# Kernel optimization log

Measured on AMD Instinct MI355X. Metric: run time of the kernel, lower is better.

Reference implementation:

```python
import jax, jax.numpy as jnp
import numpy as np

H = 64  # hidden_size hardcoded in the module


def _lstm_scan(x_pre, w_hh):
    # x_pre: [T, B, 4H] = x @ W_ih^T + b_ih + b_hh, precomputed for all steps
    # w_hh: [4H, H]. PyTorch gate order: i, f, g, o.
    B = x_pre.shape[1]
    h0 = jnp.zeros((B, H), x_pre.dtype)
    c0 = jnp.zeros((B, H), x_pre.dtype)

    def cell(carry, xp):
        h, c = carry
        gates = xp + h @ w_hh.T  # [B, 4H]
        i, f, g, o = jnp.split(gates, 4, axis=-1)
        i = jax.nn.sigmoid(i)
        f = jax.nn.sigmoid(f)
        g = jnp.tanh(g)
        o = jax.nn.sigmoid(o)
        c = f * c + i * g
        h = o * jnp.tanh(c)
        return (h, c), h

    _, hs = jax.lax.scan(cell, (h0, c0), x_pre)
    return hs  # [T, B, H]


def _bidir_layer(x, w_ih, w_hh, b_ih, b_hh):
    # x: [T, B, D]; w_ih: [2, 4H, D]; w_hh: [2, 4H, H]; b_*: [2, 4H]
    pre_f = jnp.einsum('tbd,gd->tbg', x, w_ih[0]) + b_ih[0] + b_hh[0]
    hs_f = _lstm_scan(pre_f, w_hh[0])
    xr = x[::-1]
    pre_b = jnp.einsum('tbd,gd->tbg', xr, w_ih[1]) + b_ih[1] + b_hh[1]
    hs_b = _lstm_scan(pre_b, w_hh[1])[::-1]  # re-reverse to align with time
    return jnp.concatenate([hs_f, hs_b], axis=-1)  # [T, B, 2H]


def setup_inputs() -> dict:
    key = jax.random.key(0)
    B, T, F = 1024, 512, 32
    ks = jax.random.split(key, 11)
    s = 1.0 / float(np.sqrt(H))  # PyTorch LSTM init: U(-1/sqrt(H), 1/sqrt(H))
    u = lambda k, shape: jax.random.uniform(k, shape, jnp.float32, -s, s)
    return dict(
        x=jax.random.normal(ks[0], (B, T, F), jnp.float32),
        w_ih0=u(ks[1], (2, 4 * H, F)),
        w_hh0=u(ks[2], (2, 4 * H, H)),
        b_ih0=u(ks[3], (2, 4 * H)),
        b_hh0=u(ks[4], (2, 4 * H)),
        w_ih1=u(ks[5], (2, 4 * H, 2 * H)),
        w_hh1=u(ks[6], (2, 4 * H, H)),
        b_ih1=u(ks[7], (2, 4 * H)),
        b_hh1=u(ks[8], (2, 4 * H)),
        fc_w=u(ks[9], (2, 2 * H)),
        fc_b=u(ks[10], (2,)),
    )


def reference(x, w_ih0, w_hh0, b_ih0, b_hh0, w_ih1, w_hh1, b_ih1, b_hh1, fc_w, fc_b):
    xt = jnp.transpose(x, (1, 0, 2))  # [T, B, F]
    h1 = _bidir_layer(xt, w_ih0, w_hh0, b_ih0, b_hh0)  # [T, B, 2H]
    h2 = _bidir_layer(h1, w_ih1, w_hh1, b_ih1, b_hh1)  # [T, B, 2H]
    last = h2[-1]  # out[:, -1, :] in batch_first layout -> [B, 2H]
    return last @ fc_w.T + fc_b  # [B, 2]
```

## Files before the change

kernel.cpp:

```cpp
#include <hip/hip_runtime.h>

#define TT 512
#define BB 1024
#define FF 32
#define HH 64
#define GG 256

__device__ float g_h1[(size_t)TT * BB * 2 * HH];
__device__ float g_pre0[(size_t)2 * TT * BB * GG];
__device__ float g_pre1[(size_t)TT * BB * GG];
__device__ float g_hf[(size_t)BB * HH];

__device__ __forceinline__ float fsigm(float x) {
    float e = __builtin_amdgcn_exp2f(x * -1.44269504088896f);
    return __builtin_amdgcn_rcpf(1.0f + e);
}
__device__ __forceinline__ float ftanh(float x) {
    float e = __builtin_amdgcn_exp2f(x * -2.88539008177793f);
    return 2.0f * __builtin_amdgcn_rcpf(1.0f + e) - 1.0f;
}
__device__ __forceinline__ float rlane(float v, int l) {
    return __int_as_float(__builtin_amdgcn_readlane(__float_as_int(v), l));
}

__global__ __launch_bounds__(256, 4) void pre_gemm0(
    const float* __restrict__ x,
    const float* __restrict__ w_ih,
    const float* __restrict__ b_ih,
    const float* __restrict__ b_hh)
{
    const int tid = threadIdx.x;
    const int b   = blockIdx.x >> 1;
    const int dir = blockIdx.x & 1;

    __shared__ __align__(16) float4 w4[8 * 256];
    __shared__ __align__(16) float xbuf[2][256];

    const float4* wsrc = (const float4*)(w_ih + ((size_t)dir * GG + tid) * FF);
#pragma unroll
    for (int kq = 0; kq < 8; ++kq) w4[kq * 256 + tid] = wsrc[kq];
    const float bias = b_ih[dir * GG + tid] + b_hh[dir * GG + tid];

    const float* xbase = x + (size_t)b * TT * FF;
    xbuf[0][tid] = xbase[tid];
    const size_t OS = (size_t)BB * GG;

    for (int tc = 0; tc < 64; ++tc) {
        const int cur = tc & 1;
        __syncthreads();

        float vnext = 0.f;
        if (tc + 1 < 64) vnext = xbase[(tc + 1) * 256 + tid];

        float a0 = bias, a1 = bias, a2 = bias, a3 = bias,
              a4 = bias, a5 = bias, a6 = bias, a7 = bias;
#pragma unroll
        for (int kq = 0; kq < 8; ++kq) {
            float4 wq = w4[kq * 256 + tid];
            const float4* xr = (const float4*)xbuf[cur];
            float4 q;
            q = xr[0 * 8 + kq]; a0 += q.x*wq.x + q.y*wq.y + q.z*wq.z + q.w*wq.w;
            q = xr[1 * 8 + kq]; a1 += q.x*wq.x + q.y*wq.y + q.z*wq.z + q.w*wq.w;
            q = xr[2 * 8 + kq]; a2 += q.x*wq.x + q.y*wq.y + q.z*wq.z + q.w*wq.w;
            q = xr[3 * 8 + kq]; a3 += q.x*wq.x + q.y*wq.y + q.z*wq.z + q.w*wq.w;
            q = xr[4 * 8 + kq]; a4 += q.x*wq.x + q.y*wq.y + q.z*wq.z + q.w*wq.w;
            q = xr[5 * 8 + kq]; a5 += q.x*wq.x + q.y*wq.y + q.z*wq.z + q.w*wq.w;
            q = xr[6 * 8 + kq]; a6 += q.x*wq.x + q.y*wq.y + q.z*wq.z + q.w*wq.w;
            q = xr[7 * 8 + kq]; a7 += q.x*wq.x + q.y*wq.y + q.z*wq.z + q.w*wq.w;
        }
        float* op = g_pre0 + (((size_t)dir * TT + tc * 8) * BB + b) * GG + tid;
        op[0] = a0; op[1 * OS] = a1; op[2 * OS] = a2; op[3 * OS] = a3;
        op[4 * OS] = a4; op[5 * OS] = a5; op[6 * OS] = a6; op[7 * OS] = a7;

        if (tc + 1 < 64) xbuf[1 - cur][tid] = vnext;
    }
}

template <int L>
__global__ __attribute__((amdgpu_flat_work_group_size(64, 64),
                          amdgpu_waves_per_eu(1, 1)))
void lstm_scan(
    const float* __restrict__ w_hh)
{
    const int l   = threadIdx.x;
    const int dir = (L == 0) ? (blockIdx.x & 1) : 0;
    const int b   = (L == 0) ? (int)(blockIdx.x >> 1) : (int)blockIdx.x;

    const float* wbase = w_hh + (size_t)dir * GG * HH;

    float4 wi[16], wf[16], wg[16], wo[16];
    {
        const float4* pi_ = (const float4*)(wbase + (size_t)(0   + l) * HH);
        const float4* pf_ = (const float4*)(wbase + (size_t)(64  + l) * HH);
        const float4* pg_ = (const float4*)(wbase + (size_t)(128 + l) * HH);
        const float4* po_ = (const float4*)(wbase + (size_t)(192 + l) * HH);
#pragma unroll
        for (int q = 0; q < 16; ++q) {
            wi[q] = pi_[q]; wf[q] = pf_[q]; wg[q] = pg_[q]; wo[q] = po_[q];
        }
    }

    const float* pre = (L == 0) ? (g_pre0 + (size_t)dir * TT * BB * GG) : g_pre1;

    float c = 0.f, h = 0.f;

    const int t0 = dir ? (TT - 1) : 0;
    const int t1 = dir ? (TT - 2) : 1;
    const float* pp0 = pre + ((size_t)t0 * BB + b) * GG;
    const float* pp1 = pre + ((size_t)t1 * BB + b) * GG;
    float ci0 = pp0[l], cf0 = pp0[64 + l], cg0 = pp0[128 + l], co0 = pp0[192 + l];
    float ci1 = pp1[l], cf1 = pp1[64 + l], cg1 = pp1[128 + l], co1 = pp1[192 + l];

#pragma unroll 2
    for (int s = 0; s < TT; ++s) {
        const int t = dir ? (TT - 1 - s) : s;

        float ni = 0.f, nf = 0.f, ng = 0.f, no_ = 0.f;
        if (s + 2 < TT) {
            const int tn = dir ? (TT - 3 - s) : (s + 2);
            const float* np = pre + ((size_t)tn * BB + b) * GG;
            ni = np[l]; nf = np[64 + l]; ng = np[128 + l]; no_ = np[192 + l];
        }

        float ai = ci0, af = cf0, ag = cg0, ao = co0;

#define STEPQ(q) do {                                                        \
        float s0 = rlane(h, 4*(q)+0), s1 = rlane(h, 4*(q)+1),                \
              s2 = rlane(h, 4*(q)+2), s3 = rlane(h, 4*(q)+3);                \
        ai += s0*wi[q].x + s1*wi[q].y + s2*wi[q].z + s3*wi[q].w;             \
        af += s0*wf[q].x + s1*wf[q].y + s2*wf[q].z + s3*wf[q].w;             \
        ag += s0*wg[q].x + s1*wg[q].y + s2*wg[q].z + s3*wg[q].w;             \
        ao += s0*wo[q].x + s1*wo[q].y + s2*wo[q].z + s3*wo[q].w;             \
    } while (0)

        STEPQ(0);  STEPQ(1);  STEPQ(2);  STEPQ(3);
        STEPQ(4);  STEPQ(5);  STEPQ(6);  STEPQ(7);
        STEPQ(8);  STEPQ(9);  STEPQ(10); STEPQ(11);
        STEPQ(12); STEPQ(13); STEPQ(14); STEPQ(15);
#undef STEPQ

        const float ig = fsigm(ai);
        const float fg = fsigm(af);
        const float gg = ftanh(ag);
        const float og = fsigm(ao);
        c = fg * c + ig * gg;
        h = og * ftanh(c);

        if (L == 0) {
            g_h1[((size_t)t * BB + b) * (2 * HH) + dir * HH + l] = h;
        } else {
            if (s == TT - 1) g_hf[(size_t)b * HH + l] = h;
        }

        ci0 = ci1; cf0 = cf1; cg0 = cg1; co0 = co1;
        ci1 = ni;  cf1 = nf;  cg1 = ng;  co1 = no_;
    }
}

__global__ __launch_bounds__(256, 2) void pre_gemm1(
    const float* __restrict__ w_ih,
    const float* __restrict__ b_ih,
    const float* __restrict__ b_hh)
{
    const int tid  = threadIdx.x;
    const int gl   = tid & 127;
    const int rg   = tid >> 7;
    const int b    = blockIdx.x >> 1;
    const int gate = (blockIdx.x & 1) * 128 + gl;

    __shared__ __align__(16) float4 w4[28 * 128];
    __shared__ __align__(16) float4 hstg[2][8 * 32];

    const float4* wsrc = (const float4*)w_ih + (size_t)gate * 32;
#pragma unroll
    for (int i = 0; i < 14; ++i) {
        int kq = rg * 14 + i;
        w4[kq * 128 + gl] = wsrc[kq];
    }
    float4 wr0 = wsrc[28], wr1 = wsrc[29], wr2 = wsrc[30], wr3 = wsrc[31];
    const float bias = b_ih[gate] + b_hh[gate];

    const int srow = tid >> 5, sq = tid & 31;
    hstg[0][srow * 32 + sq] =
        *((const float4*)(g_h1 + ((size_t)srow * BB + b) * 128) + sq);

    const size_t RS = (size_t)BB * GG;

    for (int tc = 0; tc < 64; ++tc) {
        const int cur = tc & 1;
        __syncthreads();

        float4 vnext = make_float4(0.f, 0.f, 0.f, 0.f);
        if (tc + 1 < 64)
            vnext = *((const float4*)(g_h1 +
                      ((size_t)((tc + 1) * 8 + srow) * BB + b) * 128) + sq);

        const float4* hr0 = &hstg[cur][(rg * 4 + 0) * 32];
        const float4* hr1 = &hstg[cur][(rg * 4 + 1) * 32];
        const float4* hr2 = &hstg[cur][(rg * 4 + 2) * 32];
        const float4* hr3 = &hstg[cur][(rg * 4 + 3) * 32];

        float a0 = bias, a1 = bias, a2 = bias, a3 = bias;
#pragma unroll
        for (int kq = 0; kq < 28; ++kq) {
            float4 wq = w4[kq * 128 + gl];
            float4 q;
            q = hr0[kq]; a0 += q.x*wq.x + q.y*wq.y + q.z*wq.z + q.w*wq.w;
            q = hr1[kq]; a1 += q.x*wq.x + q.y*wq.y + q.z*wq.z + q.w*wq.w;
            q = hr2[kq]; a2 += q.x*wq.x + q.y*wq.y + q.z*wq.z + q.w*wq.w;
            q = hr3[kq]; a3 += q.x*wq.x + q.y*wq.y + q.z*wq.z + q.w*wq.w;
        }
        {
            float4 q;
            q = hr0[28]; a0 += q.x*wr0.x + q.y*wr0.y + q.z*wr0.z + q.w*wr0.w;
            q = hr1[28]; a1 += q.x*wr0.x + q.y*wr0.y + q.z*wr0.z + q.w*wr0.w;
            q = hr2[28]; a2 += q.x*wr0.x + q.y*wr0.y + q.z*wr0.z + q.w*wr0.w;
            q = hr3[28]; a3 += q.x*wr0.x + q.y*wr0.y + q.z*wr0.z + q.w*wr0.w;
            q = hr0[29]; a0 += q.x*wr1.x + q.y*wr1.y + q.z*wr1.z + q.w*wr1.w;
            q = hr1[29]; a1 += q.x*wr1.x + q.y*wr1.y + q.z*wr1.z + q.w*wr1.w;
            q = hr2[29]; a2 += q.x*wr1.x + q.y*wr1.y + q.z*wr1.z + q.w*wr1.w;
            q = hr3[29]; a3 += q.x*wr1.x + q.y*wr1.y + q.z*wr1.z + q.w*wr1.w;
            q = hr0[30]; a0 += q.x*wr2.x + q.y*wr2.y + q.z*wr2.z + q.w*wr2.w;
            q = hr1[30]; a1 += q.x*wr2.x + q.y*wr2.y + q.z*wr2.z + q.w*wr2.w;
            q = hr2[30]; a2 += q.x*wr2.x + q.y*wr2.y + q.z*wr2.z + q.w*wr2.w;
            q = hr3[30]; a3 += q.x*wr2.x + q.y*wr2.y + q.z*wr2.z + q.w*wr2.w;
            q = hr0[31]; a0 += q.x*wr3.x + q.y*wr3.y + q.z*wr3.z + q.w*wr3.w;
            q = hr1[31]; a1 += q.x*wr3.x + q.y*wr3.y + q.z*wr3.z + q.w*wr3.w;
            q = hr2[31]; a2 += q.x*wr3.x + q.y*wr3.y + q.z*wr3.z + q.w*wr3.w;
            q = hr3[31]; a3 += q.x*wr3.x + q.y*wr3.y + q.z*wr3.z + q.w*wr3.w;
        }
        {
            const int tb = tc * 8 + rg * 4;
            float* op = g_pre1 + ((size_t)tb * BB + b) * GG + gate;
            op[0 * RS] = a0; op[1 * RS] = a1; op[2 * RS] = a2; op[3 * RS] = a3;
        }
        if (tc + 1 < 64) hstg[1 - cur][srow * 32 + sq] = vnext;
    }
}

#define FMAC4(W, P0, P1, P2, P3, K) do{                                   \
    float4 v_;                                                           \
    v_ = (P0)[K]; acc0 += W.x*v_.x; acc0 += W.y*v_.y; acc0 += W.z*v_.z; acc0 += W.w*v_.w; \
    v_ = (P1)[K]; acc1 += W.x*v_.x; acc1 += W.y*v_.y; acc1 += W.z*v_.z; acc1 += W.w*v_.w; \
    v_ = (P2)[K]; acc2 += W.x*v_.x; acc2 += W.y*v_.y; acc2 += W.z*v_.z; acc2 += W.w*v_.w; \
    v_ = (P3)[K]; acc3 += W.x*v_.x; acc3 += W.y*v_.y; acc3 += W.z*v_.z; acc3 += W.w*v_.w; \
}while(0)

__global__ __launch_bounds__(256, 2) void lstm_final(
    const float* __restrict__ w_ih,
    const float* __restrict__ b_ih,
    const float* __restrict__ b_hh,
    const float* __restrict__ fc_w,
    const float* __restrict__ fc_b,
    float* __restrict__ out)
{
    const int tid = threadIdx.x;
    const int b0  = blockIdx.x * 4;

    __shared__ __align__(16) float x_lds[4][128];
    __shared__ __align__(16) float gact[4][GG];
    __shared__ __align__(16) float last[4][128];

#pragma unroll
    for (int r = 0; r < 2; ++r) {
        int idx = tid + r * 256;
        int b = idx >> 7, col = idx & 127;
        x_lds[b][col] = g_h1[((size_t)(TT - 1) * BB + (b0 + b)) * 128 + col];
    }

    const float4* p = (const float4*)(w_ih + ((size_t)GG + tid) * 128);
    float4 w0 = p[0],  w1 = p[1],  w2 = p[2],  w3 = p[3],  w4 = p[4],  w5 = p[5],
           w6 = p[6],  w7 = p[7],  w8 = p[8],  w9 = p[9],  w10 = p[10], w11 = p[11],
           w12 = p[12], w13 = p[13], w14 = p[14], w15 = p[15], w16 = p[16], w17 = p[17],
           w18 = p[18], w19 = p[19], w20 = p[20], w21 = p[21], w22 = p[22], w23 = p[23],
           w24 = p[24], w25 = p[25], w26 = p[26], w27 = p[27], w28 = p[28], w29 = p[29],
           w30 = p[30], w31 = p[31];
    const float bias = b_ih[GG + tid] + b_hh[GG + tid];
    __syncthreads();

    const float4* xb0 = (const float4*)x_lds[0];
    const float4* xb1 = (const float4*)x_lds[1];
    const float4* xb2 = (const float4*)x_lds[2];
    const float4* xb3 = (const float4*)x_lds[3];

    float acc0 = bias, acc1 = bias, acc2 = bias, acc3 = bias;
    FMAC4(w0, xb0, xb1, xb2, xb3, 0);   FMAC4(w1, xb0, xb1, xb2, xb3, 1);
    FMAC4(w2, xb0, xb1, xb2, xb3, 2);   FMAC4(w3, xb0, xb1, xb2, xb3, 3);
    FMAC4(w4, xb0, xb1, xb2, xb3, 4);   FMAC4(w5, xb0, xb1, xb2, xb3, 5);
    FMAC4(w6, xb0, xb1, xb2, xb3, 6);   FMAC4(w7, xb0, xb1, xb2, xb3, 7);
    FMAC4(w8, xb0, xb1, xb2, xb3, 8);   FMAC4(w9, xb0, xb1, xb2, xb3, 9);
    FMAC4(w10, xb0, xb1, xb2, xb3, 10); FMAC4(w11, xb0, xb1, xb2, xb3, 11);
    FMAC4(w12, xb0, xb1, xb2, xb3, 12); FMAC4(w13, xb0, xb1, xb2, xb3, 13);
    FMAC4(w14, xb0, xb1, xb2, xb3, 14); FMAC4(w15, xb0, xb1, xb2, xb3, 15);
    FMAC4(w16, xb0, xb1, xb2, xb3, 16); FMAC4(w17, xb0, xb1, xb2, xb3, 17);
    FMAC4(w18, xb0, xb1, xb2, xb3, 18); FMAC4(w19, xb0, xb1, xb2, xb3, 19);
    FMAC4(w20, xb0, xb1, xb2, xb3, 20); FMAC4(w21, xb0, xb1, xb2, xb3, 21);
    FMAC4(w22, xb0, xb1, xb2, xb3, 22); FMAC4(w23, xb0, xb1, xb2, xb3, 23);
    FMAC4(w24, xb0, xb1, xb2, xb3, 24); FMAC4(w25, xb0, xb1, xb2, xb3, 25);
    FMAC4(w26, xb0, xb1, xb2, xb3, 26); FMAC4(w27, xb0, xb1, xb2, xb3, 27);
    FMAC4(w28, xb0, xb1, xb2, xb3, 28); FMAC4(w29, xb0, xb1, xb2, xb3, 29);
    FMAC4(w30, xb0, xb1, xb2, xb3, 30); FMAC4(w31, xb0, xb1, xb2, xb3, 31);

    const bool is_g = ((tid >> 6) == 2);
    gact[0][tid] = is_g ? ftanh(acc0) : fsigm(acc0);
    gact[1][tid] = is_g ? ftanh(acc1) : fsigm(acc1);
    gact[2][tid] = is_g ? ftanh(acc2) : fsigm(acc2);
    gact[3][tid] = is_g ? ftanh(acc3) : fsigm(acc3);
    __syncthreads();

    {
        const int cb = tid >> 6, cj = tid & 63;
        float ig = gact[cb][cj];
        float gg = gact[cb][2 * HH + cj];
        float og = gact[cb][3 * HH + cj];
        float c = ig * gg;
        float h = og * ftanh(c);
        last[cb][HH + cj] = h;
        last[cb][cj] = g_hf[(size_t)(b0 + cb) * HH + cj];
    }
    __syncthreads();

    if (tid < 8) {
        int b = tid >> 1, o = tid & 1;
        float a = fc_b[o];
#pragma unroll
        for (int j = 0; j < 128; ++j) a += fc_w[o * 128 + j] * last[b][j];
        out[(size_t)(b0 + b) * 2 + o] = a;
    }
}

extern "C" void kernel_launch(void* const* d_in, const int* in_sizes, int n_in,
                              void* d_out, int out_size, void* d_ws, size_t ws_size,
                              hipStream_t stream) {
    const float* x     = (const float*)d_in[0];
    const float* w_ih0 = (const float*)d_in[1];
    const float* w_hh0 = (const float*)d_in[2];
    const float* b_ih0 = (const float*)d_in[3];
    const float* b_hh0 = (const float*)d_in[4];
    const float* w_ih1 = (const float*)d_in[5];
    const float* w_hh1 = (const float*)d_in[6];
    const float* b_ih1 = (const float*)d_in[7];
    const float* b_hh1 = (const float*)d_in[8];
    const float* fc_w  = (const float*)d_in[9];
    const float* fc_b  = (const float*)d_in[10];
    float* out = (float*)d_out;

    pre_gemm0<<<2048, 256, 0, stream>>>(x, w_ih0, b_ih0, b_hh0);
    lstm_scan<0><<<2048, 64, 0, stream>>>(w_hh0);
    pre_gemm1<<<2048, 256, 0, stream>>>(w_ih1, b_ih1, b_hh1);
    lstm_scan<1><<<1024, 64, 0, stream>>>(w_hh1);
    lstm_final<<<256, 256, 0, stream>>>(w_ih1, b_ih1, b_hh1, fc_w, fc_b, out);
}
```

Baseline: 2.923 ms.

## Store recurrent weights in AGPRs and process two batch rows per layer-0 wave

The recurrent weight matrix rows are moved from VGPRs into accumulation registers (AGPRs) via inline asm, and read back into VGPRs just before use. The freed VGPRs let each layer-0 wave run two batch sequences at once, so one weight read feeds two dot products and the layer-0 grid is halved. This adds accvgpr read traffic to every step and removes the unroll-by-2 of the time loop. Layer 1 keeps one sequence per wave but still pays the AGPR read overhead.

Result: slower. 3.130 ms (+7.1%).

```diff
diff --git a/kernel.cpp b/kernel.cpp
--- a/kernel.cpp
+++ b/kernel.cpp
@@ -76,61 +76,130 @@
     }
 }
 
+#define AQD(p) float p##_x, p##_y, p##_z, p##_w
+#define AQW(p, src4) do { float4 q_ = (src4);                                  \
+    asm volatile("v_accvgpr_write_b32 %0, %1" : "=a"(p##_x) : "v"(q_.x));      \
+    asm volatile("v_accvgpr_write_b32 %0, %1" : "=a"(p##_y) : "v"(q_.y));      \
+    asm volatile("v_accvgpr_write_b32 %0, %1" : "=a"(p##_z) : "v"(q_.z));      \
+    asm volatile("v_accvgpr_write_b32 %0, %1" : "=a"(p##_w) : "v"(q_.w));      \
+} while (0)
+#define AQR(p) do {                                                            \
+    asm volatile("v_accvgpr_read_b32 %0, %1" : "=v"(wx) : "a"(p##_x));         \
+    asm volatile("v_accvgpr_read_b32 %0, %1" : "=v"(wy) : "a"(p##_y));         \
+    asm volatile("v_accvgpr_read_b32 %0, %1" : "=v"(wz) : "a"(p##_z));         \
+    asm volatile("v_accvgpr_read_b32 %0, %1" : "=v"(ww) : "a"(p##_w));         \
+} while (0)
+
 template <int L>
 __global__ __attribute__((amdgpu_flat_work_group_size(64, 64),
                           amdgpu_waves_per_eu(1, 1)))
 void lstm_scan(
     const float* __restrict__ w_hh)
 {
+    constexpr bool B2 = (L == 0);
     const int l   = threadIdx.x;
     const int dir = (L == 0) ? (blockIdx.x & 1) : 0;
-    const int b   = (L == 0) ? (int)(blockIdx.x >> 1) : (int)blockIdx.x;
+    const int b0  = (L == 0) ? (int)(blockIdx.x >> 1) * 2 : (int)blockIdx.x;
+    const int b1  = b0 + 1;
 
     const float* wbase = w_hh + (size_t)dir * GG * HH;
 
-    float4 wi[16], wf[16], wg[16], wo[16];
-    {
-        const float4* pi_ = (const float4*)(wbase + (size_t)(0   + l) * HH);
-        const float4* pf_ = (const float4*)(wbase + (size_t)(64  + l) * HH);
-        const float4* pg_ = (const float4*)(wbase + (size_t)(128 + l) * HH);
-        const float4* po_ = (const float4*)(wbase + (size_t)(192 + l) * HH);
-#pragma unroll
-        for (int q = 0; q < 16; ++q) {
-            wi[q] = pi_[q]; wf[q] = pf_[q]; wg[q] = pg_[q]; wo[q] = po_[q];
-        }
-    }
+    const float4* pi_ = (const float4*)(wbase + (size_t)(0   + l) * HH);
+    const float4* pf_ = (const float4*)(wbase + (size_t)(64  + l) * HH);
+    const float4* pg_ = (const float4*)(wbase + (size_t)(128 + l) * HH);
+    const float4* po_ = (const float4*)(wbase + (size_t)(192 + l) * HH);
+
+    AQD(wi0);  AQD(wi1);  AQD(wi2);  AQD(wi3);
+    AQD(wi4);  AQD(wi5);  AQD(wi6);  AQD(wi7);
+    AQD(wi8);  AQD(wi9);  AQD(wi10); AQD(wi11);
+    AQD(wi12); AQD(wi13); AQD(wi14); AQD(wi15);
+    AQD(wf0);  AQD(wf1);  AQD(wf2);  AQD(wf3);
+    AQD(wf4);  AQD(wf5);  AQD(wf6);  AQD(wf7);
+    AQD(wf8);  AQD(wf9);  AQD(wf10); AQD(wf11);
+    AQD(wf12); AQD(wf13); AQD(wf14); AQD(wf15);
+    AQD(wg0);  AQD(wg1);  AQD(wg2);  AQD(wg3);
+    AQD(wg4);  AQD(wg5);  AQD(wg6);  AQD(wg7);
+    AQD(wg8);  AQD(wg9);  AQD(wg10); AQD(wg11);
+    AQD(wg12); AQD(wg13); AQD(wg14); AQD(wg15);
+    AQD(wo0);  AQD(wo1);  AQD(wo2);  AQD(wo3);
+    AQD(wo4);  AQD(wo5);  AQD(wo6);  AQD(wo7);
+    AQD(wo8);  AQD(wo9);  AQD(wo10); AQD(wo11);
+    AQD(wo12); AQD(wo13); AQD(wo14); AQD(wo15);
+
+    AQW(wi0,  pi_[0]);  AQW(wi1,  pi_[1]);  AQW(wi2,  pi_[2]);  AQW(wi3,  pi_[3]);
+    AQW(wi4,  pi_[4]);  AQW(wi5,  pi_[5]);  AQW(wi6,  pi_[6]);  AQW(wi7,  pi_[7]);
+    AQW(wi8,  pi_[8]);  AQW(wi9,  pi_[9]);  AQW(wi10, pi_[10]); AQW(wi11, pi_[11]);
+    AQW(wi12, pi_[12]); AQW(wi13, pi_[13]); AQW(wi14, pi_[14]); AQW(wi15, pi_[15]);
+    AQW(wf0,  pf_[0]);  AQW(wf1,  pf_[1]);  AQW(wf2,  pf_[2]);  AQW(wf3,  pf_[3]);
+    AQW(wf4,  pf_[4]);  AQW(wf5,  pf_[5]);  AQW(wf6,  pf_[6]);  AQW(wf7,  pf_[7]);
+    AQW(wf8,  pf_[8]);  AQW(wf9,  pf_[9]);  AQW(wf10, pf_[10]); AQW(wf11, pf_[11]);
+    AQW(wf12, pf_[12]); AQW(wf13, pf_[13]); AQW(wf14, pf_[14]); AQW(wf15, pf_[15]);
+    AQW(wg0,  pg_[0]);  AQW(wg1,  pg_[1]);  AQW(wg2,  pg_[2]);  AQW(wg3,  pg_[3]);
+    AQW(wg4,  pg_[4]);  AQW(wg5,  pg_[5]);  AQW(wg6,  pg_[6]);  AQW(wg7,  pg_[7]);
+    AQW(wg8,  pg_[8]);  AQW(wg9,  pg_[9]);  AQW(wg10, pg_[10]); AQW(wg11, pg_[11]);
+    AQW(wg12, pg_[12]); AQW(wg13, pg_[13]); AQW(wg14, pg_[14]); AQW(wg15, pg_[15]);
+    AQW(wo0,  po_[0]);  AQW(wo1,  po_[1]);  AQW(wo2,  po_[2]);  AQW(wo3,  po_[3]);
+    AQW(wo4,  po_[4]);  AQW(wo5,  po_[5]);  AQW(wo6,  po_[6]);  AQW(wo7,  po_[7]);
+    AQW(wo8,  po_[8]);  AQW(wo9,  po_[9]);  AQW(wo10, po_[10]); AQW(wo11, po_[11]);
+    AQW(wo12, po_[12]); AQW(wo13, po_[13]); AQW(wo14, po_[14]); AQW(wo15, po_[15]);
 
     const float* pre = (L == 0) ? (g_pre0 + (size_t)dir * TT * BB * GG) : g_pre1;
 
-    float c = 0.f, h = 0.f;
+    float c0 = 0.f, h0 = 0.f, c1 = 0.f, h1 = 0.f;
 
     const int t0 = dir ? (TT - 1) : 0;
     const int t1 = dir ? (TT - 2) : 1;
-    const float* pp0 = pre + ((size_t)t0 * BB + b) * GG;
-    const float* pp1 = pre + ((size_t)t1 * BB + b) * GG;
-    float ci0 = pp0[l], cf0 = pp0[64 + l], cg0 = pp0[128 + l], co0 = pp0[192 + l];
-    float ci1 = pp1[l], cf1 = pp1[64 + l], cg1 = pp1[128 + l], co1 = pp1[192 + l];
-
-#pragma unroll 2
+    const float* pp0a = pre + ((size_t)t0 * BB + b0) * GG;
+    const float* pp1a = pre + ((size_t)t1 * BB + b0) * GG;
+    float p_i0 = pp0a[l], p_f0 = pp0a[64 + l], p_g0 = pp0a[128 + l], p_o0 = pp0a[192 + l];
+    float n_i0 = pp1a[l], n_f0 = pp1a[64 + l], n_g0 = pp1a[128 + l], n_o0 = pp1a[192 + l];
+    float p_i1 = 0.f, p_f1 = 0.f, p_g1 = 0.f, p_o1 = 0.f;
+    float n_i1 = 0.f, n_f1 = 0.f, n_g1 = 0.f, n_o1 = 0.f;
+    if (B2) {
+        const float* pp0b = pre + ((size_t)t0 * BB + b1) * GG;
+        const float* pp1b = pre + ((size_t)t1 * BB + b1) * GG;
+        p_i1 = pp0b[l]; p_f1 = pp0b[64 + l]; p_g1 = pp0b[128 + l]; p_o1 = pp0b[192 + l];
+        n_i1 = pp1b[l]; n_f1 = pp1b[64 + l]; n_g1 = pp1b[128 + l]; n_o1 = pp1b[192 + l];
+    }
+
+#pragma unroll 1
     for (int s = 0; s < TT; ++s) {
         const int t = dir ? (TT - 1 - s) : s;
 
-        float ni = 0.f, nf = 0.f, ng = 0.f, no_ = 0.f;
+        float f_i0 = 0.f, f_f0 = 0.f, f_g0 = 0.f, f_o0 = 0.f;
+        float f_i1 = 0.f, f_f1 = 0.f, f_g1 = 0.f, f_o1 = 0.f;
         if (s + 2 < TT) {
             const int tn = dir ? (TT - 3 - s) : (s + 2);
-            const float* np = pre + ((size_t)tn * BB + b) * GG;
-            ni = np[l]; nf = np[64 + l]; ng = np[128 + l]; no_ = np[192 + l];
-        }
-
-        float ai = ci0, af = cf0, ag = cg0, ao = co0;
-
-#define STEPQ(q) do {                                                        \
-        float s0 = rlane(h, 4*(q)+0), s1 = rlane(h, 4*(q)+1),                \
-              s2 = rlane(h, 4*(q)+2), s3 = rlane(h, 4*(q)+3);                \
-        ai += s0*wi[q].x + s1*wi[q].y + s2*wi[q].z + s3*wi[q].w;             \
-        af += s0*wf[q].x + s1*wf[q].y + s2*wf[q].z + s3*wf[q].w;             \
-        ag += s0*wg[q].x + s1*wg[q].y + s2*wg[q].z + s3*wg[q].w;             \
-        ao += s0*wo[q].x + s1*wo[q].y + s2*wo[q].z + s3*wo[q].w;             \
+            const float* np0 = pre + ((size_t)tn * BB + b0) * GG;
+            f_i0 = np0[l]; f_f0 = np0[64 + l]; f_g0 = np0[128 + l]; f_o0 = np0[192 + l];
+            if (B2) {
+                const float* np1 = pre + ((size_t)tn * BB + b1) * GG;
+                f_i1 = np1[l]; f_f1 = np1[64 + l]; f_g1 = np1[128 + l]; f_o1 = np1[192 + l];
+            }
+        }
+
+        float ai0 = p_i0, af0 = p_f0, ag0 = p_g0, ao0 = p_o0;
+        float ai1 = p_i1, af1 = p_f1, ag1 = p_g1, ao1 = p_o1;
+
+#define STEPQ(q) do {                                                          \
+        float wx, wy, wz, ww;                                                  \
+        const float s0 = rlane(h0, 4*q+0), s1 = rlane(h0, 4*q+1),              \
+                    s2 = rlane(h0, 4*q+2), s3 = rlane(h0, 4*q+3);              \
+        float u0 = 0.f, u1 = 0.f, u2 = 0.f, u3 = 0.f;                          \
+        if (B2) { u0 = rlane(h1, 4*q+0); u1 = rlane(h1, 4*q+1);                \
+                  u2 = rlane(h1, 4*q+2); u3 = rlane(h1, 4*q+3); }              \
+        AQR(wi##q);                                                            \
+        ai0 += s0*wx + s1*wy + s2*wz + s3*ww;                                  \
+        if (B2) ai1 += u0*wx + u1*wy + u2*wz + u3*ww;                          \
+        AQR(wf##q);                                                            \
+        af0 += s0*wx + s1*wy + s2*wz + s3*ww;                                  \
+        if (B2) af1 += u0*wx + u1*wy + u2*wz + u3*ww;                          \
+        AQR(wg##q);                                                            \
+        ag0 += s0*wx + s1*wy + s2*wz + s3*ww;                                  \
+        if (B2) ag1 += u0*wx + u1*wy + u2*wz + u3*ww;                          \
+        AQR(wo##q);                                                            \
+        ao0 += s0*wx + s1*wy + s2*wz + s3*ww;                                  \
+        if (B2) ao1 += u0*wx + u1*wy + u2*wz + u3*ww;                          \
     } while (0)
 
         STEPQ(0);  STEPQ(1);  STEPQ(2);  STEPQ(3);
@@ -139,21 +208,33 @@
         STEPQ(12); STEPQ(13); STEPQ(14); STEPQ(15);
 #undef STEPQ
 
-        const float ig = fsigm(ai);
-        const float fg = fsigm(af);
-        const float gg = ftanh(ag);
-        const float og = fsigm(ao);
-        c = fg * c + ig * gg;
-        h = og * ftanh(c);
+        {
+            const float ig = fsigm(ai0), fg = fsigm(af0),
+                        gg = ftanh(ag0), og = fsigm(ao0);
+            c0 = fg * c0 + ig * gg;
+            h0 = og * ftanh(c0);
+        }
+        if (B2) {
+            const float ig = fsigm(ai1), fg = fsigm(af1),
+                        gg = ftanh(ag1), og = fsigm(ao1);
+            c1 = fg * c1 + ig * gg;
+            h1 = og * ftanh(c1);
+        }
 
         if (L == 0) {
-            g_h1[((size_t)t * BB + b) * (2 * HH) + dir * HH + l] = h;
+            g_h1[((size_t)t * BB + b0) * (2 * HH) + dir * HH + l] = h0;
+            if (B2)
+                g_h1[((size_t)t * BB + b1) * (2 * HH) + dir * HH + l] = h1;
         } else {
-            if (s == TT - 1) g_hf[(size_t)b * HH + l] = h;
-        }
-
-        ci0 = ci1; cf0 = cf1; cg0 = cg1; co0 = co1;
-        ci1 = ni;  cf1 = nf;  cg1 = ng;  co1 = no_;
+            if (s == TT - 1) g_hf[(size_t)b0 * HH + l] = h0;
+        }
+
+        p_i0 = n_i0; p_f0 = n_f0; p_g0 = n_g0; p_o0 = n_o0;
+        n_i0 = f_i0; n_f0 = f_f0; n_g0 = f_g0; n_o0 = f_o0;
+        if (B2) {
+            p_i1 = n_i1; p_f1 = n_f1; p_g1 = n_g1; p_o1 = n_o1;
+            n_i1 = f_i1; n_f1 = f_f1; n_g1 = f_g1; n_o1 = f_o1;
+        }
     }
 }
 
@@ -346,7 +427,7 @@
     float* out = (float*)d_out;
 
     pre_gemm0<<<2048, 256, 0, stream>>>(x, w_ih0, b_ih0, b_hh0);
-    lstm_scan<0><<<2048, 64, 0, stream>>>(w_hh0);
+    lstm_scan<0><<<1024, 64, 0, stream>>>(w_hh0);
     pre_gemm1<<<2048, 256, 0, stream>>>(w_ih1, b_ih1, b_hh1);
     lstm_scan<1><<<1024, 64, 0, stream>>>(w_hh1);
     lstm_final<<<256, 256, 0, stream>>>(w_ih1, b_ih1, b_hh1, fc_w, fc_b, out);
```
